# Performance work log

Hardware: AMD Instinct MI355X
Metric: run time of the kernel (lower is better)

## Reference

```python
import jax, jax.numpy as jnp
import numpy as np

EMB = 3          # embedding_size
NSIG = 1         # n_sigma
FG_W = 1.0       # foreground_weight
W_INST, W_VAR, W_SEED = 1.0, 10.0, 1.0
K_MAX = 8        # fixed number of instance ids (1..K_MAX); 0 is background


def _xyzm(T, H, W):
    # buffer is linspace over the FULL grid (32,800,2000), then sliced
    t = jnp.linspace(0.0, 0.1, 32)[:T]
    y = jnp.linspace(0.0, 1.6, 800)[:H]
    x = jnp.linspace(0.0, 4.16, 2000)[:W]
    tt = jnp.broadcast_to(t[:, None, None], (T, H, W))
    yy = jnp.broadcast_to(y[None, :, None], (T, H, W))
    xx = jnp.broadcast_to(x[None, None, :], (T, H, W))
    return jnp.stack([tt, yy, xx], 0)  # [3,T,H,W]


def _lovasz_hinge_flat(logits, labels):
    # standard Berman lovasz hinge on flat [N] logits/labels (labels in {0,1})
    signs = 2.0 * labels - 1.0
    errors = 1.0 - logits * signs
    order = jnp.argsort(-errors)             # descending errors
    errors_sorted = errors[order]
    gt_sorted = labels[order]
    gts = gt_sorted.sum()
    inter = gts - jnp.cumsum(gt_sorted)
    union = gts + jnp.cumsum(1.0 - gt_sorted)
    jac = 1.0 - inter / union
    grad = jnp.concatenate([jac[:1], jac[1:] - jac[:-1]])
    return jnp.dot(jax.nn.relu(errors_sorted), jax.lax.stop_gradient(grad))


def _forward(prediction, instances):
    B, C, T, H, W = prediction.shape
    xyzm = _xyzm(T, H, W).astype(prediction.dtype)

    emb = jnp.tanh(prediction[:, :EMB])                 # [B,3,T,H,W]
    spatial = emb + xyzm[None]                          # spatial_emb
    sigma = prediction[:, EMB]                          # [B,T,H,W] (n_sigma=1)
    seed = jax.nn.sigmoid(prediction[:, EMB + NSIG])    # [B,T,H,W]

    ids = jnp.arange(1, K_MAX + 1)
    masks = (instances[:, None] == ids[None, :, None, None, None]).astype(prediction.dtype)  # [B,K,T,H,W]
    counts = masks.sum((2, 3, 4))                       # [B,K]
    present = (counts > 0).astype(prediction.dtype)
    safe = jnp.maximum(counts, 1.0)

    # per-instance center of xyzm (to_center=True) and mean sigma
    centers = jnp.einsum('cthw,bkthw->bkc', xyzm, masks) / safe[..., None]   # [B,K,3]
    s_mean = jnp.einsum('bthw,bkthw->bk', sigma, masks) / safe               # [B,K]
    s_sg = jax.lax.stop_gradient(s_mean)

    # var loss: mean over mask of (sigma - stop_grad(s_mean))^2
    sig2 = jnp.einsum('bthw,bkthw->bk', sigma * sigma, masks) / safe
    var_k = sig2 - 2.0 * s_sg * s_mean + s_sg * s_sg                          # [B,K]

    # gaussian distance map: exp(-s * ||spatial - center||^2)
    s_exp = jnp.exp(s_mean * 10.0)                                            # [B,K]
    e2 = jnp.sum(spatial * spatial, axis=1)                                   # [B,T,H,W]
    ec = jnp.einsum('bcthw,bkc->bkthw', spatial, centers)                     # [B,K,T,H,W]
    c2 = jnp.sum(centers * centers, axis=-1)                                  # [B,K]
    sqdist = e2[:, None] - 2.0 * ec + c2[:, :, None, None, None]
    dist = jnp.exp(-s_exp[:, :, None, None, None] * sqdist)                   # [B,K,T,H,W]

    # lovasz hinge per instance
    logits = (dist * 2.0 - 1.0).reshape(B * K_MAX, -1)
    labels_flat = masks.reshape(B * K_MAX, -1)
    inst_k = jax.vmap(_lovasz_hinge_flat)(logits, labels_flat).reshape(B, K_MAX)

    obj = present.sum(1)
    safe_obj = jnp.maximum(obj, 1.0)
    inst_loss = (inst_k * present).sum(1) / safe_obj
    var_loss = (var_k * present).sum(1) / safe_obj

    # seed loss: background -> 0, foreground -> stop_grad(dist)
    bg = (instances == 0).astype(prediction.dtype)
    seed_bg = jnp.sum(bg * seed * seed, axis=(1, 2, 3))
    dsg = jax.lax.stop_gradient(dist)
    seed_fg = FG_W * jnp.sum(masks * (seed[:, None] - dsg) ** 2, axis=(1, 2, 3, 4))
    seed_loss = (seed_bg + seed_fg) / (H * W)

    return jnp.mean(W_INST * inst_loss + W_VAR * var_loss + W_SEED * seed_loss)


def setup_inputs() -> dict:
    key = jax.random.key(0)
    k1, k2, k3 = jax.random.split(key, 3)
    prediction = jax.random.normal(k1, (2, 5, 8, 256, 512), dtype=jnp.float32)
    instances = jax.random.randint(k2, (2, 8, 256, 512), 0, 9, dtype=jnp.int32)
    labels = jax.random.randint(k3, (2, 8, 256, 512), 0, 2, dtype=jnp.int32)
    return {"prediction": prediction, "instances": instances, "labels": labels}


def reference(prediction, instances, labels):
    # `labels` is accepted by the torch forward but unused in the loss math
    return _forward(prediction, instances)
```

## Files before the change

kernel.cpp:

```cpp
#include <hip/hip_runtime.h>
#include <math.h>

#define BB 2
#define KK 8
#define NB 256
#define HALF_NB_F 128.0f
#define FAR_CUT 5.545177444479562f

#define PXB_H 2048
#define GRID_H 1024
#define GRID_A 256
#define NPART_A 128

#define STEP_T (0.1f/31.0f)
#define STEP_Y (1.6f/799.0f)
#define STEP_X (4.16f/1999.0f)

#define OFF_CNT 0
#define OFF_PRM 32
#define OFF_GH2 512
#define OFF_PARTA 9216
#define OFF_SEED2 25600
#define OFF_HIST_F 32768

typedef float nvf4 __attribute__((ext_vector_type(4)));
typedef int   nvi4 __attribute__((ext_vector_type(4)));

__device__ __forceinline__ float4 ntload4f(const float* p) {
  nvf4 v = __builtin_nontemporal_load((const nvf4*)p);
  return make_float4(v.x, v.y, v.z, v.w);
}
__device__ __forceinline__ int4 ntload4i(const int* p) {
  nvi4 v = __builtin_nontemporal_load((const nvi4*)p);
  return make_int4(v.x, v.y, v.z, v.w);
}

__global__ __launch_bounds__(512) void k_acc(const float* __restrict__ pred,
                                             const int* __restrict__ inst,
                                             float* __restrict__ ws) {
  int tid = threadIdx.x, blk = blockIdx.x;
  int b = blk >> 7;
  int rbase = (blk & 127) * 8192;
  const float* sig_p = pred + ((size_t)b * 5 << 20) + (3 << 20);
  const int* ip = inst + ((size_t)b << 20);
  float acc[48];
  #pragma unroll
  for (int f = 0; f < 48; ++f) acc[f] = 0.f;
  #pragma unroll
  for (int it = 0; it < 4; ++it) {
    int r = rbase + it * 2048 + 4 * tid;
    float4 sg4 = ntload4f(sig_p + r);
    int4 id4 = ntload4i(ip + r);
    float tf = (float)(r >> 17), hf = (float)((r >> 9) & 255), wf = (float)(r & 511);
    float sv[4] = {sg4.x, sg4.y, sg4.z, sg4.w};
    int iv[4] = {id4.x, id4.y, id4.z, id4.w};
    #pragma unroll
    for (int j = 0; j < 4; ++j) {
      #pragma unroll
      for (int k = 0; k < KK; ++k) {
        float m = (iv[j] == k + 1) ? 1.f : 0.f;
        acc[k*6+0] += m;
        acc[k*6+1] += m * sv[j];
        acc[k*6+2] += m * sv[j] * sv[j];
        acc[k*6+3] += m * tf;
        acc[k*6+4] += m * hf;
        acc[k*6+5] += m * (wf + (float)j);
      }
    }
  }
  __shared__ float lds[8 * 48];
  int lane = tid & 63, wv = tid >> 6;
  #pragma unroll
  for (int f = 0; f < 48; ++f) {
    float v = acc[f];
    for (int o = 32; o; o >>= 1) v += __shfl_down(v, o);
    if (lane == 0) lds[wv * 48 + f] = v;
  }
  __syncthreads();
  if (tid < 48) {
    float s = 0.f;
    #pragma unroll
    for (int w8 = 0; w8 < 8; ++w8) s += lds[w8 * 48 + tid];
    ws[OFF_PARTA + ((size_t)b * 48 + tid) * NPART_A + (blk & 127)] = s;
  }
}

__device__ __forceinline__ float fast_tanh(float x) {
  x = fminf(fmaxf(x, -15.f), 15.f);
  float ex = __expf(2.f * x);
  return (ex - 1.f) / (ex + 1.f);
}

__global__ __launch_bounds__(512, 8) void k_hist(const float* __restrict__ pred,
                                                 const int* __restrict__ inst,
                                                 float* __restrict__ ws) {
  __shared__ unsigned int hist[KK * NB];
  __shared__ float fred[48 * 8];
  __shared__ float accs[48];
  __shared__ float Ps[KK * 8];
  __shared__ float wred[16];
  int tid = threadIdx.x;
  int blk = blockIdx.x;
  int b = blk >> 9;
  for (int i = tid; i < KK * NB; i += 512) hist[i] = 0u;
  if (tid < 384) {
    int f = tid >> 3, g = tid & 7;
    const float* p = ws + OFF_PARTA + ((size_t)b * 48 + f) * NPART_A + g * 16;
    float s = 0.f;
    #pragma unroll
    for (int j = 0; j < 16; ++j) s += p[j];
    fred[f * 8 + g] = s;
  }
  __syncthreads();
  if (tid < 48) {
    const float* q = &fred[tid * 8];
    accs[tid] = ((q[0]+q[1])+(q[2]+q[3])) + ((q[4]+q[5])+(q[6]+q[7]));
  }
  __syncthreads();
  if (tid < 8) {
    const float* a = &accs[tid * 6];
    float cnt = a[0], s1 = a[1], s2 = a[2], st = a[3], sy = a[4], sx = a[5];
    float safe = fmaxf(cnt, 1.f);
    float smean = s1 / safe;
    float A = __expf(10.f * smean);
    float ct = st * STEP_T / safe;
    float cy = sy * STEP_Y / safe;
    float cx = sx * STEP_X / safe;
    float var = s2 / safe - smean * smean;
    float pres = (cnt > 0.f) ? 1.f : 0.f;
    Ps[tid*8 + 0] = 2.f * A * ct;
    Ps[tid*8 + 1] = 2.f * A * cy;
    Ps[tid*8 + 2] = 2.f * A * cx;
    Ps[tid*8 + 3] = A;
    Ps[tid*8 + 4] = A * (ct*ct + cy*cy + cx*cx);
    Ps[tid*8 + 5] = pres;
    if ((blk & 511) == 0) {
      int seg = b * 8 + tid;
      ws[OFF_CNT + seg] = cnt;
      ws[OFF_PRM + seg*8 + 5] = var;
      ws[OFF_PRM + seg*8 + 6] = pres;
    }
  }
  __syncthreads();
  unsigned pmask = 0;
  #pragma unroll
  for (int k = 0; k < KK; ++k) if (Ps[k*8 + 5] > 0.f) pmask |= 1u << k;
  int r = (blk & 511) * PXB_H + 4 * tid;
  const float* pb = pred + ((size_t)b * 5 << 20);
  float tf = (float)(r >> 17), hf = (float)((r >> 9) & 255);
  int w = r & 511;
  float4 p0 = ntload4f(pb + r);
  float4 p1 = ntload4f(pb + (1 << 20) + r);
  float4 p2 = ntload4f(pb + (2 << 20) + r);
  float4 p4 = ntload4f(pb + (4 << 20) + r);
  int4 id4 = ntload4i(inst + ((size_t)b << 20) + r);
  int iv[4] = {id4.x, id4.y, id4.z, id4.w};
  float e0[4], e1[4], e2[4], ee[4], sd[4];
  {
    float q0[4] = {p0.x,p0.y,p0.z,p0.w}, q1[4] = {p1.x,p1.y,p1.z,p1.w};
    float q2[4] = {p2.x,p2.y,p2.z,p2.w}, q4[4] = {p4.x,p4.y,p4.z,p4.w};
    #pragma unroll
    for (int j = 0; j < 4; ++j) {
      e0[j] = fast_tanh(q0[j]) + tf * STEP_T;
      e1[j] = fast_tanh(q1[j]) + hf * STEP_Y;
      e2[j] = fast_tanh(q2[j]) + (float)(w + j) * STEP_X;
      ee[j] = e0[j]*e0[j] + e1[j]*e1[j] + e2[j]*e2[j];
      sd[j] = 1.f / (1.f + __expf(-q4[j]));
    }
  }
  float sbg = 0.f, sfg = 0.f;
  #pragma unroll
  for (int j = 0; j < 4; ++j) if (iv[j] == 0) sbg += sd[j] * sd[j];
  int lane = tid & 63;
  unsigned hot[KK];
  #pragma unroll
  for (int k = 0; k < KK; ++k) hot[k] = 0u;
  #pragma unroll
  for (int k = 0; k < KK; ++k) {
    if (!((pmask >> k) & 1)) continue;
    float Bt = Ps[k*8+0], By = Ps[k*8+1], Bx = Ps[k*8+2], A = Ps[k*8+3], C = Ps[k*8+4];
    #pragma unroll
    for (int j = 0; j < 4; ++j) {
      float ssq = fmaf(-Bt, e0[j], fmaf(-By, e1[j], fmaf(-Bx, e2[j], fmaf(A, ee[j], C))));
      bool lab = (iv[j] == k + 1);
      if (ssq >= FAR_CUT) {
        hot[k] += lab ? 0x10000u : 1u;
        if (lab) sfg += sd[j] * sd[j];
      } else {
        float d = __expf(-ssq);
        float e;
        if (lab) { float df = sd[j] - d; sfg += df * df; e = 2.f - 2.f * d; }
        else e = 2.f * d;
        int bin = min((int)(e * HALF_NB_F), NB - 1);
        atomicAdd(&hist[k * NB + bin], lab ? 0x10000u : 1u);
      }
    }
  }
  #pragma unroll
  for (int k = 0; k < KK; ++k) {
    unsigned v = hot[k];
    for (int o = 32; o; o >>= 1) v += __shfl_down(v, o);
    if (lane == 0 && v) {
      unsigned neg = v & 0xFFFFu, pos = v & 0xFFFF0000u;
      if (neg) atomicAdd(&hist[k * NB], neg);
      if (pos) atomicAdd(&hist[k * NB + NB - 1], pos);
    }
  }
  for (int off = 32; off; off >>= 1) {
    sbg += __shfl_down(sbg, off);
    sfg += __shfl_down(sfg, off);
  }
  if (lane == 0) { wred[(tid >> 6) * 2] = sbg; wred[(tid >> 6) * 2 + 1] = sfg; }
  __syncthreads();
  if (tid == 0) {
    float b0 = 0.f, f0 = 0.f;
    #pragma unroll
    for (int v = 0; v < 8; ++v) { b0 += wred[v*2]; f0 += wred[v*2+1]; }
    ((float2*)(ws + OFF_SEED2))[blk] = make_float2(b0, f0);
  }
  uint4* gp = (uint4*)((unsigned int*)(ws + OFF_HIST_F) + (size_t)blk * (KK * NB));
  gp[tid] = ((const uint4*)hist)[tid];
}

__global__ __launch_bounds__(256) void k_red(float* __restrict__ ws) {
  int blk = blockIdx.x;
  int tid = threadIdx.x;
  int seg = blk >> 4, range = blk & 15;
  int b = seg >> 3, k = seg & 7;
  __shared__ unsigned long long sred[256];
  int bin_off = tid & 15;
  int pgrp = tid >> 4;
  const unsigned int* gh = (const unsigned int*)(ws + OFF_HIST_F);
  size_t base = ((size_t)b * 512 + (size_t)pgrp * 32) * (KK * NB)
              + (size_t)k * NB + (size_t)range * 16 + bin_off;
  unsigned int neg = 0, pos = 0;
  #pragma unroll 4
  for (int j = 0; j < 32; ++j) {
    unsigned v = gh[base + (size_t)j * (KK * NB)];
    neg += v & 0xFFFFu; pos += v >> 16;
  }
  sred[tid] = ((unsigned long long)pos << 32) | neg;
  __syncthreads();
  if (tid < 16) {
    unsigned long long a = 0;
    #pragma unroll
    for (int j = 0; j < 16; ++j) a += sred[tid + j * 16];
    ((unsigned long long*)(ws + OFF_GH2))[seg * NB + range * 16 + tid] = a;
  }
}

__global__ __launch_bounds__(256) void k_fin(float* __restrict__ ws, float* __restrict__ out) {
  int tid = threadIdx.x;
  int lane = tid & 63, wv = tid >> 6;
  __shared__ double segtot[16];
  __shared__ float sdb[4], sdf[4];
  {
    const float2* sp = (const float2*)(ws + OFF_SEED2);
    float sb = 0.f, sf = 0.f;
    #pragma unroll
    for (int j = 0; j < 4; ++j) { float2 v = sp[tid * 4 + j]; sb += v.x; sf += v.y; }
    for (int o = 32; o; o >>= 1) { sb += __shfl_down(sb, o); sf += __shfl_down(sf, o); }
    if (lane == 0) { sdb[wv] = sb; sdf[wv] = sf; }
  }
  const unsigned long long* gh2 = (const unsigned long long*)(ws + OFF_GH2);
  for (int s = wv; s < 16; s += 4) {
    double total = 0.0;
    if (ws[OFF_PRM + s*8 + 6] != 0.f) {
      double gts = (double)ws[OFF_CNT + s];
      unsigned long long carry = 0;
      double sum = 0.0;
      for (int c = 0; c < NB / 64; ++c) {
        int bin = NB - 1 - (c * 64 + lane);
        unsigned long long v = gh2[s * NB + bin];
        unsigned long long orig = v;
        #pragma unroll
        for (int o = 1; o < 64; o <<= 1) {
          unsigned long long u = (unsigned long long)__shfl_up((long long)v, o, 64);
          if (lane >= o) v += u;
        }
        v += carry;
        if (orig) {
          unsigned int ip = (unsigned)(v >> 32), in_ = (unsigned)v;
          unsigned int ppx = (unsigned)(orig >> 32), nnx = (unsigned)orig;
          double ep = (double)(ip - ppx), en = (double)(in_ - nnx);
          double js = 1.0 - (gts - ep) / (gts + en);
          double je = 1.0 - (gts - (double)ip) / (gts + (double)in_);
          sum += ((double)bin + 0.5) * (2.0 / NB) * (je - js);
        }
        carry = (unsigned long long)__shfl((long long)v, 63, 64);
      }
      for (int o = 32; o; o >>= 1) sum += __shfl_down(sum, o);
      total = sum;
    }
    if (lane == 0) segtot[s] = total;
  }
  __syncthreads();
  if (tid == 0) {
    double tot = 0.0;
    for (int bb = 0; bb < BB; ++bb) {
      double il = 0.0, vl = 0.0, ob = 0.0;
      for (int k2 = 0; k2 < KK; ++k2) {
        int s2 = bb * 8 + k2;
        double pr = (double)ws[OFF_PRM + s2*8 + 6];
        il += segtot[s2] * pr;
        vl += (double)ws[OFF_PRM + s2*8 + 5] * pr;
        ob += pr;
      }
      double so = (ob > 1.0) ? ob : 1.0;
      double sbg = (double)sdb[bb * 2] + (double)sdb[bb * 2 + 1];
      double sfg = (double)sdf[bb * 2] + (double)sdf[bb * 2 + 1];
      tot += il / so + 10.0 * vl / so + (sbg + sfg) / (256.0 * 512.0);
    }
    out[0] = (float)(tot / BB);
  }
}

extern "C" void kernel_launch(void* const* d_in, const int* in_sizes, int n_in,
                              void* d_out, int out_size, void* d_ws, size_t ws_size,
                              hipStream_t stream) {
  const float* pred = (const float*)d_in[0];
  const int* inst = (const int*)d_in[1];
  float* ws = (float*)d_ws;
  float* out = (float*)d_out;
  k_acc<<<GRID_A, 512, 0, stream>>>(pred, inst, ws);
  k_hist<<<GRID_H, 512, 0, stream>>>(pred, inst, ws);
  k_red<<<256, 256, 0, stream>>>(ws);
  k_fin<<<1, 256, 0, stream>>>(ws, out);
}
```

Before: 137.4 us.

## Widen k_acc grid and move Lovasz scan into per-segment histogram reduction

k_acc now runs 1024 blocks of 256 threads with fewer pixels each, which raises parallelism in the first pass, and k_hist reads four times as many partials. The histogram reduction and the Lovasz cumulative scan are merged into k_red, with one block per (batch, instance) segment plus one extra block for the seed sums. Segments whose instance is absent skip their work early. k_fin shrinks to a trivial combine. The risk is that only 16 blocks each loop serially over 512 partial histograms, which could make that stage latency-bound and lose the earlier 256-block parallel reduction.

```diff
diff --git a/kernel.cpp b/kernel.cpp
--- a/kernel.cpp
+++ b/kernel.cpp
@@ -9,8 +9,8 @@
 
 #define PXB_H 2048
 #define GRID_H 1024
-#define GRID_A 256
-#define NPART_A 128
+#define GRID_A 1024
+#define NPART_A 512
 
 #define STEP_T (0.1f/31.0f)
 #define STEP_Y (1.6f/799.0f)
@@ -18,10 +18,11 @@
 
 #define OFF_CNT 0
 #define OFF_PRM 32
-#define OFF_GH2 512
+#define OFF_SEGT 512
+#define OFF_SEEDT 560
 #define OFF_PARTA 9216
-#define OFF_SEED2 25600
-#define OFF_HIST_F 32768
+#define OFF_SEED2 58880
+#define OFF_HIST_F 65536
 
 typedef float nvf4 __attribute__((ext_vector_type(4)));
 typedef int   nvi4 __attribute__((ext_vector_type(4)));
@@ -35,20 +36,20 @@
   return make_int4(v.x, v.y, v.z, v.w);
 }
 
-__global__ __launch_bounds__(512) void k_acc(const float* __restrict__ pred,
-                                             const int* __restrict__ inst,
-                                             float* __restrict__ ws) {
+__global__ __launch_bounds__(256, 4) void k_acc(const float* __restrict__ pred,
+                                                const int* __restrict__ inst,
+                                                float* __restrict__ ws) {
   int tid = threadIdx.x, blk = blockIdx.x;
-  int b = blk >> 7;
-  int rbase = (blk & 127) * 8192;
+  int b = blk >> 9;
+  int rbase = (blk & 511) * 2048;
   const float* sig_p = pred + ((size_t)b * 5 << 20) + (3 << 20);
   const int* ip = inst + ((size_t)b << 20);
   float acc[48];
   #pragma unroll
   for (int f = 0; f < 48; ++f) acc[f] = 0.f;
   #pragma unroll
-  for (int it = 0; it < 4; ++it) {
-    int r = rbase + it * 2048 + 4 * tid;
+  for (int it = 0; it < 2; ++it) {
+    int r = rbase + it * 1024 + 4 * tid;
     float4 sg4 = ntload4f(sig_p + r);
     int4 id4 = ntload4i(ip + r);
     float tf = (float)(r >> 17), hf = (float)((r >> 9) & 255), wf = (float)(r & 511);
@@ -68,7 +69,7 @@
       }
     }
   }
-  __shared__ float lds[8 * 48];
+  __shared__ float lds[4 * 48];
   int lane = tid & 63, wv = tid >> 6;
   #pragma unroll
   for (int f = 0; f < 48; ++f) {
@@ -77,12 +78,9 @@
     if (lane == 0) lds[wv * 48 + f] = v;
   }
   __syncthreads();
-  if (tid < 48) {
-    float s = 0.f;
-    #pragma unroll
-    for (int w8 = 0; w8 < 8; ++w8) s += lds[w8 * 48 + tid];
-    ws[OFF_PARTA + ((size_t)b * 48 + tid) * NPART_A + (blk & 127)] = s;
-  }
+  if (tid < 48)
+    ws[OFF_PARTA + ((size_t)b * 48 + tid) * NPART_A + (blk & 511)]
+      = (lds[tid] + lds[48 + tid]) + (lds[96 + tid] + lds[144 + tid]);
 }
 
 __device__ __forceinline__ float fast_tanh(float x) {
@@ -105,10 +103,10 @@
   for (int i = tid; i < KK * NB; i += 512) hist[i] = 0u;
   if (tid < 384) {
     int f = tid >> 3, g = tid & 7;
-    const float* p = ws + OFF_PARTA + ((size_t)b * 48 + f) * NPART_A + g * 16;
+    const float* p = ws + OFF_PARTA + ((size_t)b * 48 + f) * NPART_A + g * 64;
     float s = 0.f;
     #pragma unroll
-    for (int j = 0; j < 16; ++j) s += p[j];
+    for (int j = 0; j < 64; ++j) s += p[j];
     fred[f * 8 + g] = s;
   }
   __syncthreads();
@@ -225,77 +223,68 @@
 __global__ __launch_bounds__(256) void k_red(float* __restrict__ ws) {
   int blk = blockIdx.x;
   int tid = threadIdx.x;
-  int seg = blk >> 4, range = blk & 15;
-  int b = seg >> 3, k = seg & 7;
-  __shared__ unsigned long long sred[256];
-  int bin_off = tid & 15;
-  int pgrp = tid >> 4;
-  const unsigned int* gh = (const unsigned int*)(ws + OFF_HIST_F);
-  size_t base = ((size_t)b * 512 + (size_t)pgrp * 32) * (KK * NB)
-              + (size_t)k * NB + (size_t)range * 16 + bin_off;
-  unsigned int neg = 0, pos = 0;
-  #pragma unroll 4
-  for (int j = 0; j < 32; ++j) {
-    unsigned v = gh[base + (size_t)j * (KK * NB)];
-    neg += v & 0xFFFFu; pos += v >> 16;
-  }
-  sred[tid] = ((unsigned long long)pos << 32) | neg;
-  __syncthreads();
-  if (tid < 16) {
-    unsigned long long a = 0;
-    #pragma unroll
-    for (int j = 0; j < 16; ++j) a += sred[tid + j * 16];
-    ((unsigned long long*)(ws + OFF_GH2))[seg * NB + range * 16 + tid] = a;
-  }
-}
-
-__global__ __launch_bounds__(256) void k_fin(float* __restrict__ ws, float* __restrict__ out) {
-  int tid = threadIdx.x;
   int lane = tid & 63, wv = tid >> 6;
-  __shared__ double segtot[16];
-  __shared__ float sdb[4], sdf[4];
-  {
+  if (blk == 16) {
+    __shared__ float sdb[4], sdf[4];
     const float2* sp = (const float2*)(ws + OFF_SEED2);
     float sb = 0.f, sf = 0.f;
     #pragma unroll
     for (int j = 0; j < 4; ++j) { float2 v = sp[tid * 4 + j]; sb += v.x; sf += v.y; }
     for (int o = 32; o; o >>= 1) { sb += __shfl_down(sb, o); sf += __shfl_down(sf, o); }
     if (lane == 0) { sdb[wv] = sb; sdf[wv] = sf; }
-  }
-  const unsigned long long* gh2 = (const unsigned long long*)(ws + OFF_GH2);
-  for (int s = wv; s < 16; s += 4) {
-    double total = 0.0;
-    if (ws[OFF_PRM + s*8 + 6] != 0.f) {
-      double gts = (double)ws[OFF_CNT + s];
-      unsigned long long carry = 0;
-      double sum = 0.0;
-      for (int c = 0; c < NB / 64; ++c) {
-        int bin = NB - 1 - (c * 64 + lane);
-        unsigned long long v = gh2[s * NB + bin];
-        unsigned long long orig = v;
-        #pragma unroll
-        for (int o = 1; o < 64; o <<= 1) {
-          unsigned long long u = (unsigned long long)__shfl_up((long long)v, o, 64);
-          if (lane >= o) v += u;
-        }
-        v += carry;
-        if (orig) {
-          unsigned int ip = (unsigned)(v >> 32), in_ = (unsigned)v;
-          unsigned int ppx = (unsigned)(orig >> 32), nnx = (unsigned)orig;
-          double ep = (double)(ip - ppx), en = (double)(in_ - nnx);
-          double js = 1.0 - (gts - ep) / (gts + en);
-          double je = 1.0 - (gts - (double)ip) / (gts + (double)in_);
-          sum += ((double)bin + 0.5) * (2.0 / NB) * (je - js);
-        }
-        carry = (unsigned long long)__shfl((long long)v, 63, 64);
-      }
-      for (int o = 32; o; o >>= 1) sum += __shfl_down(sum, o);
-      total = sum;
-    }
-    if (lane == 0) segtot[s] = total;
-  }
-  __syncthreads();
-  if (tid == 0) {
+    __syncthreads();
+    if (tid < 2)
+      ((float2*)(ws + OFF_SEEDT))[tid] =
+        make_float2(sdb[tid*2] + sdb[tid*2+1], sdf[tid*2] + sdf[tid*2+1]);
+    return;
+  }
+  int seg = blk, b = seg >> 3, k = seg & 7;
+  if (ws[OFF_PRM + seg*8 + 6] == 0.f) {
+    if (tid == 0) ((double*)(ws + OFF_SEGT))[seg] = 0.0;
+    return;
+  }
+  const unsigned int* gh = (const unsigned int*)(ws + OFF_HIST_F) + (size_t)b * 512 * (KK*NB) + k * NB;
+  unsigned int neg = 0, pos = 0;
+  for (int p = 0; p < 512; ++p) {
+    unsigned v = gh[(size_t)p * (KK * NB) + tid];
+    neg += v & 0xFFFFu; pos += v >> 16;
+  }
+  __shared__ unsigned long long binc[NB];
+  binc[tid] = ((unsigned long long)pos << 32) | neg;
+  __syncthreads();
+  if (wv == 0) {
+    double gts = (double)ws[OFF_CNT + seg];
+    unsigned long long carry = 0;
+    double sum = 0.0;
+    for (int c = 0; c < NB / 64; ++c) {
+      int bin = NB - 1 - (c * 64 + lane);
+      unsigned long long v = binc[bin];
+      unsigned long long orig = v;
+      #pragma unroll
+      for (int o = 1; o < 64; o <<= 1) {
+        unsigned long long u = (unsigned long long)__shfl_up((long long)v, o, 64);
+        if (lane >= o) v += u;
+      }
+      v += carry;
+      if (orig) {
+        unsigned int ip = (unsigned)(v >> 32), in_ = (unsigned)v;
+        unsigned int ppx = (unsigned)(orig >> 32), nnx = (unsigned)orig;
+        double ep = (double)(ip - ppx), en = (double)(in_ - nnx);
+        double js = 1.0 - (gts - ep) / (gts + en);
+        double je = 1.0 - (gts - (double)ip) / (gts + (double)in_);
+        sum += ((double)bin + 0.5) * (2.0 / NB) * (je - js);
+      }
+      carry = (unsigned long long)__shfl((long long)v, 63, 64);
+    }
+    for (int o = 32; o; o >>= 1) sum += __shfl_down(sum, o);
+    if (lane == 0) ((double*)(ws + OFF_SEGT))[seg] = sum;
+  }
+}
+
+__global__ __launch_bounds__(64) void k_fin(const float* __restrict__ ws, float* __restrict__ out) {
+  if (threadIdx.x == 0) {
+    const double* segtot = (const double*)(ws + OFF_SEGT);
+    const float2* seedt = (const float2*)(ws + OFF_SEEDT);
     double tot = 0.0;
     for (int bb = 0; bb < BB; ++bb) {
       double il = 0.0, vl = 0.0, ob = 0.0;
@@ -307,9 +296,8 @@
         ob += pr;
       }
       double so = (ob > 1.0) ? ob : 1.0;
-      double sbg = (double)sdb[bb * 2] + (double)sdb[bb * 2 + 1];
-      double sfg = (double)sdf[bb * 2] + (double)sdf[bb * 2 + 1];
-      tot += il / so + 10.0 * vl / so + (sbg + sfg) / (256.0 * 512.0);
+      float2 st = seedt[bb];
+      tot += il / so + 10.0 * vl / so + ((double)st.x + (double)st.y) / (256.0 * 512.0);
     }
     out[0] = (float)(tot / BB);
   }
@@ -322,8 +310,8 @@
   const int* inst = (const int*)d_in[1];
   float* ws = (float*)d_ws;
   float* out = (float*)d_out;
-  k_acc<<<GRID_A, 512, 0, stream>>>(pred, inst, ws);
+  k_acc<<<GRID_A, 256, 0, stream>>>(pred, inst, ws);
   k_hist<<<GRID_H, 512, 0, stream>>>(pred, inst, ws);
-  k_red<<<256, 256, 0, stream>>>(ws);
-  k_fin<<<1, 256, 0, stream>>>(ws, out);
-}
+  k_red<<<17, 256, 0, stream>>>(ws);
+  k_fin<<<1, 64, 0, stream>>>(ws, out);
+}
```

Measured after the change: 159.8 us. 16.3% more time.
